# Performance work log

Measured on AMD Instinct MI355X. Metric: run time of the kernel, lower is better.

The kernel has to match this reference:

```python
import jax, jax.numpy as jnp
import numpy as np

N_NODES = 6144
IN_FEATURES = 256
N_HEADS = 4
N_HIDDEN = 64  # out_features, concat=False
LEAKY_SLOPE = 0.2
NEG_INF = -9e16


def setup_inputs() -> dict:
    key = jax.random.key(0)
    k1, k2, k3, k4 = jax.random.split(key, 4)
    h = jax.random.normal(k1, (N_NODES, IN_FEATURES), dtype=jnp.float32)
    adj_mat = jax.random.randint(k2, (N_NODES, N_NODES), 0, 2, dtype=jnp.int32)
    W = jax.random.normal(k3, (IN_FEATURES, N_HEADS * N_HIDDEN), dtype=jnp.float32) * 0.06
    a = jax.random.normal(k4, (N_HEADS, 2 * N_HIDDEN, 1), dtype=jnp.float32) * 0.1
    return {"h": h, "adj_mat": adj_mat, "W": W, "a": a}


def reference(h, adj_mat, W, a):
    n_nodes = h.shape[0]
    # linear transform, dropout is identity in eval mode
    ht = (h @ W).reshape(n_nodes, N_HEADS, N_HIDDEN).transpose(1, 0, 2)  # [H, N, d]
    a_src = a[:, :N_HIDDEN, 0]   # [H, d]
    a_tgt = a[:, N_HIDDEN:, 0]   # [H, d]
    src = jnp.einsum('hnd,hd->hn', ht, a_src)  # [H, N]
    tgt = jnp.einsum('hnd,hd->hn', ht, a_tgt)  # [H, N]
    e = src[:, :, None] + tgt[:, None, :]       # [H, N, N]
    e = jnp.where(e >= 0, e, LEAKY_SLOPE * e)    # leaky relu
    e = jnp.where(adj_mat[None, :, :] > 0, e, jnp.float32(NEG_INF))
    attention = jax.nn.softmax(e, axis=-1)       # [H, N, N]
    h_prime = jnp.einsum('hij,hjd->hid', attention, ht)  # [H, N, d]
    return h_prime.mean(axis=0)                  # [N, d] (concat=False)
```

## Files before the change

kernel.cpp:

```cpp
#include <hip/hip_runtime.h>
#include <hip/hip_bf16.h>

#define N_NODES 6144
#define IN_F 256
#define N_HEADS 4
#define N_HID 64
#define JS 4
#define JLEN (N_NODES / JS)
#define NW (JLEN / 32)
#define SMB_STRIDE 1544

typedef __attribute__((ext_vector_type(4))) float floatx4;
typedef _Float16 half2_t __attribute__((ext_vector_type(2)));
typedef _Float16 half8_t __attribute__((ext_vector_type(8)));
typedef __attribute__((ext_vector_type(4))) unsigned uint4_t;

__global__ __launch_bounds__(256) void ht_gemm_kernel(
    const float* __restrict__ h, const float* __restrict__ W,
    const float* __restrict__ a, short* __restrict__ htF,
    float* __restrict__ srcv, unsigned* __restrict__ tE1pk, unsigned* __restrict__ tE2pk)
{
    __shared__ float As[32][34];
    __shared__ float Bs[32][68];
    __shared__ float redS[32][16];
    __shared__ float redT[32][16];
    __shared__ unsigned short eh1[32], eh2[32];

    const int head = blockIdx.y;
    const int i0 = blockIdx.x * 32;
    const int tid = threadIdx.x;
    const int tx = tid & 15, ty = tid >> 4;

    float acc[2][4] = {};

    for (int k0 = 0; k0 < IN_F; k0 += 32) {
        __syncthreads();
        {
            const int m = tid >> 3, kq = tid & 7;
            const float4 v = *(const float4*)(h + (i0 + m) * IN_F + k0 + kq * 4);
            As[kq*4+0][m] = v.x; As[kq*4+1][m] = v.y;
            As[kq*4+2][m] = v.z; As[kq*4+3][m] = v.w;
        }
        #pragma unroll
        for (int it = 0; it < 2; ++it) {
            int l = it * 256 + tid;
            int k = l >> 4, nq = l & 15;
            *(float4*)&Bs[k][nq*4] = *(const float4*)(W + (k0 + k) * 256 + head * 64 + nq * 4);
        }
        __syncthreads();
        #pragma unroll
        for (int kk = 0; kk < 32; ++kk) {
            const float2 av = *(const float2*)&As[kk][ty*2];
            const float4 bv = *(const float4*)&Bs[kk][tx*4];
            const float aa[2] = {av.x, av.y};
            const float bb[4] = {bv.x, bv.y, bv.z, bv.w};
            #pragma unroll
            for (int r = 0; r < 2; ++r)
                #pragma unroll
                for (int c = 0; c < 4; ++c)
                    acc[r][c] = fmaf(aa[r], bb[c], acc[r][c]);
        }
    }

    #pragma unroll
    for (int r = 0; r < 2; ++r)
        #pragma unroll
        for (int c2 = 0; c2 < 4; ++c2) {
            const int d = tx * 4 + c2;
            const int j = i0 + ty * 2 + r;
            const int jt = j >> 5, q = (j >> 3) & 3, u = j & 7;
            const int c = d >> 4, n = d & 15;
            const size_t F = (((((size_t)head * 192 + jt) * 4 + c) * 16 + n) * 4 + q) * 8 + u;
            const _Float16 hv = (_Float16)acc[r][c2];
            htF[F] = *(const short*)&hv;
        }

    float as_[4], at_[4];
    #pragma unroll
    for (int c = 0; c < 4; ++c) {
        as_[c] = a[head * 128 + tx * 4 + c];
        at_[c] = a[head * 128 + 64 + tx * 4 + c];
    }
    #pragma unroll
    for (int r = 0; r < 2; ++r) {
        float ps = 0.f, pt = 0.f;
        #pragma unroll
        for (int c = 0; c < 4; ++c) {
            ps = fmaf(acc[r][c], as_[c], ps);
            pt = fmaf(acc[r][c], at_[c], pt);
        }
        redS[ty*2+r][tx] = ps;
        redT[ty*2+r][tx] = pt;
    }
    __syncthreads();
    if (tid < 64) {
        const int row = tid & 31;
        const float* src = (tid < 32) ? &redS[row][0] : &redT[row][0];
        float s = 0.f;
        #pragma unroll
        for (int x = 0; x < 16; ++x) s += src[x];
        if (tid < 32) {
            srcv[head * N_NODES + i0 + row] = s;
        } else {
            const _Float16 E1 = (_Float16)__expf(s);
            const _Float16 E2 = (_Float16)__expf(0.2f * s);
            eh1[row] = *(const unsigned short*)&E1;
            eh2[row] = *(const unsigned short*)&E2;
        }
    }
    __syncthreads();
    if (tid < 16) {
        const unsigned v1 = (unsigned)eh1[2*tid] | ((unsigned)eh1[2*tid+1] << 16);
        const unsigned v2 = (unsigned)eh2[2*tid] | ((unsigned)eh2[2*tid+1] << 16);
        tE1pk[head * (N_NODES/2) + i0/2 + tid] = v1;
        tE2pk[head * (N_NODES/2) + i0/2 + tid] = v2;
    }
}

__global__ __launch_bounds__(256) void gat_main_kernel(
    const int* __restrict__ adj, const short* __restrict__ htF,
    const float* __restrict__ srcv, const unsigned* __restrict__ tE1pk,
    const unsigned* __restrict__ tE2pk,
    float* __restrict__ pnum, float* __restrict__ pden)
{
    __shared__ unsigned char smaskB[16 * SMB_STRIDE];

    const int lane = threadIdx.x;
    const int head = threadIdx.y;
    const int jc = blockIdx.y;
    const int i0 = blockIdx.x * 16;
    const int m = lane & 15, quad = lane >> 4;
    const int row = i0 + m;
    const int jbase = jc * JLEN;

    const int tid = head * 64 + lane;
    #pragma unroll
    for (int it = 0; it < 24; ++it) {
        const int flat = it * 256 + tid;
        const int r = flat / 384;
        const int c4 = flat - r * 384;
        const int4 v = *(const int4*)(adj + (size_t)(i0 + r) * N_NODES + jbase + c4 * 4);
        const unsigned b = (unsigned)(v.x | (v.y << 8) | (v.z << 16) | (v.w << 24)) * 255u;
        *(unsigned*)(smaskB + r * SMB_STRIDE + c4 * 4) = b;
    }
    __syncthreads();

    const float sv = srcv[head * N_NODES + row];
    const _Float16 e1h = (_Float16)__expf(sv);
    const _Float16 e2h = (_Float16)__expf(0.2f * sv);
    const half2_t e1s2 = {e1h, e1h};
    const half2_t e2s2 = {e2h, e2h};

    const unsigned* pe1 = tE1pk + head * (N_NODES/2) + (jbase >> 1);
    const unsigned* pe2 = tE2pk + head * (N_NODES/2) + (jbase >> 1);
    const short* fb = htF + ((size_t)(head * 192 + (jbase >> 5)) * 4) * 512 + (m * 4 + quad) * 8;

    half8_t bones;
    #pragma unroll
    for (int u = 0; u < 8; ++u) bones[u] = (_Float16)1.0f;

    floatx4 acc0 = {0,0,0,0}, acc1 = {0,0,0,0}, acc2 = {0,0,0,0}, acc3 = {0,0,0,0};
    floatx4 accD = {0,0,0,0};

    for (int w = 0; w < NW; ++w) {
        const uint4_t E1 = *(const uint4_t*)(pe1 + w * 16 + quad * 4);
        const uint4_t E2 = *(const uint4_t*)(pe2 + w * 16 + quad * 4);
        const unsigned long long mB =
            *(const unsigned long long*)(smaskB + m * SMB_STRIDE + w * 32 + quad * 8);
        const unsigned mlo = (unsigned)mB, mhi = (unsigned)(mB >> 32);

        const half8_t b0 = *(const half8_t*)(fb + (size_t)w * 2048);
        const half8_t b1 = *(const half8_t*)(fb + (size_t)w * 2048 + 512);
        const half8_t b2 = *(const half8_t*)(fb + (size_t)w * 2048 + 1024);
        const half8_t b3 = *(const half8_t*)(fb + (size_t)w * 2048 + 1536);

        const unsigned k0 = __builtin_amdgcn_perm(0u, mlo, 0x01010000u);
        const unsigned k1 = __builtin_amdgcn_perm(0u, mlo, 0x03030202u);
        const unsigned k2 = __builtin_amdgcn_perm(0u, mhi, 0x01010000u);
        const unsigned k3 = __builtin_amdgcn_perm(0u, mhi, 0x03030202u);

        uint4_t af_u;
        #pragma unroll
        for (int p = 0; p < 4; ++p) {
            const unsigned e1u = (p == 0) ? E1.x : (p == 1) ? E1.y : (p == 2) ? E1.z : E1.w;
            const unsigned e2u = (p == 0) ? E2.x : (p == 1) ? E2.y : (p == 2) ? E2.z : E2.w;
            const unsigned ku  = (p == 0) ? k0 : (p == 1) ? k1 : (p == 2) ? k2 : k3;
            const half2_t p1 = __builtin_bit_cast(half2_t, e1u) * e1s2;
            const half2_t p2 = __builtin_bit_cast(half2_t, e2u) * e2s2;
            const half2_t mx = __builtin_elementwise_max(p1, p2);
            const unsigned r = __builtin_bit_cast(unsigned, mx) & ku;
            if (p == 0) af_u.x = r; else if (p == 1) af_u.y = r;
            else if (p == 2) af_u.z = r; else af_u.w = r;
        }
        const half8_t af = __builtin_bit_cast(half8_t, af_u);

        acc0 = __builtin_amdgcn_mfma_f32_16x16x32_f16(af, b0, acc0, 0, 0, 0);
        acc1 = __builtin_amdgcn_mfma_f32_16x16x32_f16(af, b1, acc1, 0, 0, 0);
        acc2 = __builtin_amdgcn_mfma_f32_16x16x32_f16(af, b2, acc2, 0, 0, 0);
        acc3 = __builtin_amdgcn_mfma_f32_16x16x32_f16(af, b3, acc3, 0, 0, 0);
        accD = __builtin_amdgcn_mfma_f32_16x16x32_f16(af, bones, accD, 0, 0, 0);
    }

    const int slot = jc * N_HEADS + head;

    if (m == 0) {
        #pragma unroll
        for (int r = 0; r < 4; ++r)
            pden[slot * N_NODES + i0 + quad * 4 + r] = accD[r];
    }

    #pragma unroll
    for (int r = 0; r < 4; ++r) {
        const int gi = i0 + quad * 4 + r;
        float* np_ = pnum + ((size_t)slot * N_NODES + gi) * N_HID + m;
        np_[0]  = acc0[r];
        np_[16] = acc1[r];
        np_[32] = acc2[r];
        np_[48] = acc3[r];
    }
}

__global__ __launch_bounds__(256) void finalize_kernel(
    const float* __restrict__ pnum, const float* __restrict__ pden,
    float* __restrict__ out)
{
    const int idx = blockIdx.x * 256 + threadIdx.x;
    if (idx >= N_NODES * N_HID) return;
    const int i = idx >> 6;
    const int d = idx & 63;
    float s = 0.f;
    for (int hh = 0; hh < N_HEADS; ++hh) {
        float ns = 0.f, ds = 0.f;
        #pragma unroll
        for (int jc = 0; jc < JS; ++jc) {
            const int slot = jc * N_HEADS + hh;
            ns += pnum[((size_t)slot * N_NODES + i) * N_HID + d];
            ds += pden[slot * N_NODES + i];
        }
        s += ns / ds;
    }
    out[idx] = 0.25f * s;
}

extern "C" void kernel_launch(void* const* d_in, const int* in_sizes, int n_in,
                              void* d_out, int out_size, void* d_ws, size_t ws_size,
                              hipStream_t stream)
{
    const float* h   = (const float*)d_in[0];
    const int*   adj = (const int*)d_in[1];
    const float* W   = (const float*)d_in[2];
    const float* a   = (const float*)d_in[3];
    float* out = (float*)d_out;

    char* ws = (char*)d_ws;
    short* htF = (short*)ws;
    size_t off = (size_t)N_HEADS * N_HID * N_NODES * 2;
    float* srcv = (float*)(ws + off);       off += (size_t)N_HEADS * N_NODES * 4;
    unsigned* tE1pk = (unsigned*)(ws + off); off += (size_t)N_HEADS * (N_NODES/2) * 4;
    unsigned* tE2pk = (unsigned*)(ws + off); off += (size_t)N_HEADS * (N_NODES/2) * 4;
    float* pnum = (float*)(ws + off);        off += (size_t)JS * N_HEADS * N_NODES * N_HID * 4;
    float* pden = (float*)(ws + off);

    ht_gemm_kernel<<<dim3(N_NODES / 32, N_HEADS), 256, 0, stream>>>(h, W, a, htF, srcv, tE1pk, tE2pk);
    gat_main_kernel<<<dim3(N_NODES / 16, JS), dim3(64, 4), 0, stream>>>(
        adj, htF, srcv, tE1pk, tE2pk, pnum, pden);
    finalize_kernel<<<dim3((N_NODES * N_HID) / 256), 256, 0, stream>>>(pnum, pden, out);
}
```

Baseline: 315.6 us.

## Prepack adjacency to bitmask and tile 64 rows per wave per head

Adds a pre-pass that packs the int32 adjacency matrix into 32-bit bitmasks. The main kernel then loads the compact mask into shared memory instead of converting raw ints per block. The main kernel is regridded so each block handles one head and 256 rows, with each wave computing four 16-row tiles. This reuses each loaded htF fragment across four MFMA row tiles. The j-split rises to 8 when workspace allows, which increases partial-sum traffic and register pressure from 20 accumulators in exchange for more parallelism and less redundant feature loading.

```diff
diff --git a/kernel.cpp b/kernel.cpp
--- a/kernel.cpp
+++ b/kernel.cpp
@@ -5,15 +5,35 @@
 #define IN_F 256
 #define N_HEADS 4
 #define N_HID 64
-#define JS 4
-#define JLEN (N_NODES / JS)
-#define NW (JLEN / 32)
-#define SMB_STRIDE 1544
+#define NWORDS (N_NODES / 32)
 
 typedef __attribute__((ext_vector_type(4))) float floatx4;
 typedef _Float16 half2_t __attribute__((ext_vector_type(2)));
 typedef _Float16 half8_t __attribute__((ext_vector_type(8)));
 typedef __attribute__((ext_vector_type(4))) unsigned uint4_t;
+typedef short short2v __attribute__((ext_vector_type(2)));
+
+__global__ __launch_bounds__(256) void pack_adj_kernel(
+    const int* __restrict__ adj, unsigned* __restrict__ mask32)
+{
+    const int waveId = (blockIdx.x * 256 + threadIdx.x) >> 6;
+    const int lane = threadIdx.x & 63;
+    #pragma unroll
+    for (int c = 0; c < 3; ++c) {
+        const size_t W = ((size_t)c * 6144 + waveId) * 64 + lane;
+        const int* p = adj + W * 32;
+        unsigned mw = 0;
+        #pragma unroll
+        for (int k = 0; k < 8; ++k) {
+            const int4 v = *(const int4*)(p + k * 4);
+            mw |= (unsigned)v.x << (k * 4 + 0);
+            mw |= (unsigned)v.y << (k * 4 + 1);
+            mw |= (unsigned)v.z << (k * 4 + 2);
+            mw |= (unsigned)v.w << (k * 4 + 3);
+        }
+        mask32[W] = mw;
+    }
+}
 
 __global__ __launch_bounds__(256) void ht_gemm_kernel(
     const float* __restrict__ h, const float* __restrict__ W,
@@ -117,122 +137,130 @@
     }
 }
 
-__global__ __launch_bounds__(256) void gat_main_kernel(
-    const int* __restrict__ adj, const short* __restrict__ htF,
+__global__ __launch_bounds__(256, 3) void gat_main_kernel(
+    const unsigned* __restrict__ mask32, const short* __restrict__ htF,
     const float* __restrict__ srcv, const unsigned* __restrict__ tE1pk,
     const unsigned* __restrict__ tE2pk,
-    float* __restrict__ pnum, float* __restrict__ pden)
-{
-    __shared__ unsigned char smaskB[16 * SMB_STRIDE];
+    float* __restrict__ pnum, float* __restrict__ pden, int nw)
+{
+    __shared__ unsigned smask[256 * 49];
 
     const int lane = threadIdx.x;
-    const int head = threadIdx.y;
+    const int wy = threadIdx.y;
     const int jc = blockIdx.y;
-    const int i0 = blockIdx.x * 16;
+    const int head = blockIdx.z;
+    const int rb0 = blockIdx.x * 256;
     const int m = lane & 15, quad = lane >> 4;
-    const int row = i0 + m;
-    const int jbase = jc * JLEN;
-
-    const int tid = head * 64 + lane;
-    #pragma unroll
-    for (int it = 0; it < 24; ++it) {
+    const int jbase = jc * nw * 32;
+
+    const int tid = wy * 64 + lane;
+    const int perThread = nw >> 2;
+    for (int it = 0; it < perThread; ++it) {
         const int flat = it * 256 + tid;
-        const int r = flat / 384;
-        const int c4 = flat - r * 384;
-        const int4 v = *(const int4*)(adj + (size_t)(i0 + r) * N_NODES + jbase + c4 * 4);
-        const unsigned b = (unsigned)(v.x | (v.y << 8) | (v.z << 16) | (v.w << 24)) * 255u;
-        *(unsigned*)(smaskB + r * SMB_STRIDE + c4 * 4) = b;
+        const int r = flat / perThread, w4 = flat % perThread;
+        const uint4_t v = *(const uint4_t*)(mask32 + (size_t)(rb0 + r) * NWORDS + jc * nw + w4 * 4);
+        unsigned* dst = &smask[r * 49 + w4 * 4];
+        dst[0] = v.x; dst[1] = v.y; dst[2] = v.z; dst[3] = v.w;
     }
     __syncthreads();
 
-    const float sv = srcv[head * N_NODES + row];
-    const _Float16 e1h = (_Float16)__expf(sv);
-    const _Float16 e2h = (_Float16)__expf(0.2f * sv);
-    const half2_t e1s2 = {e1h, e1h};
-    const half2_t e2s2 = {e2h, e2h};
+    const int rowbase = rb0 + wy * 64;
+    half2_t e1s[4], e2s[4];
+    #pragma unroll
+    for (int t = 0; t < 4; ++t) {
+        const float sv = srcv[head * N_NODES + rowbase + t * 16 + m];
+        const _Float16 a1 = (_Float16)__expf(sv);
+        const _Float16 a2 = (_Float16)__expf(0.2f * sv);
+        e1s[t] = (half2_t){a1, a1};
+        e2s[t] = (half2_t){a2, a2};
+    }
 
     const unsigned* pe1 = tE1pk + head * (N_NODES/2) + (jbase >> 1);
     const unsigned* pe2 = tE2pk + head * (N_NODES/2) + (jbase >> 1);
     const short* fb = htF + ((size_t)(head * 192 + (jbase >> 5)) * 4) * 512 + (m * 4 + quad) * 8;
+    const unsigned* mrow = &smask[(wy * 64 + m) * 49];
 
     half8_t bones;
     #pragma unroll
     for (int u = 0; u < 8; ++u) bones[u] = (_Float16)1.0f;
 
-    floatx4 acc0 = {0,0,0,0}, acc1 = {0,0,0,0}, acc2 = {0,0,0,0}, acc3 = {0,0,0,0};
-    floatx4 accD = {0,0,0,0};
-
-    for (int w = 0; w < NW; ++w) {
+    floatx4 accN[4][4];
+    floatx4 accD[4];
+    #pragma unroll
+    for (int t = 0; t < 4; ++t) {
+        accD[t] = (floatx4){0,0,0,0};
+        #pragma unroll
+        for (int c = 0; c < 4; ++c) accN[t][c] = (floatx4){0,0,0,0};
+    }
+
+    for (int w = 0; w < nw; ++w) {
         const uint4_t E1 = *(const uint4_t*)(pe1 + w * 16 + quad * 4);
         const uint4_t E2 = *(const uint4_t*)(pe2 + w * 16 + quad * 4);
-        const unsigned long long mB =
-            *(const unsigned long long*)(smaskB + m * SMB_STRIDE + w * 32 + quad * 8);
-        const unsigned mlo = (unsigned)mB, mhi = (unsigned)(mB >> 32);
-
-        const half8_t b0 = *(const half8_t*)(fb + (size_t)w * 2048);
-        const half8_t b1 = *(const half8_t*)(fb + (size_t)w * 2048 + 512);
-        const half8_t b2 = *(const half8_t*)(fb + (size_t)w * 2048 + 1024);
-        const half8_t b3 = *(const half8_t*)(fb + (size_t)w * 2048 + 1536);
-
-        const unsigned k0 = __builtin_amdgcn_perm(0u, mlo, 0x01010000u);
-        const unsigned k1 = __builtin_amdgcn_perm(0u, mlo, 0x03030202u);
-        const unsigned k2 = __builtin_amdgcn_perm(0u, mhi, 0x01010000u);
-        const unsigned k3 = __builtin_amdgcn_perm(0u, mhi, 0x03030202u);
-
-        uint4_t af_u;
-        #pragma unroll
-        for (int p = 0; p < 4; ++p) {
-            const unsigned e1u = (p == 0) ? E1.x : (p == 1) ? E1.y : (p == 2) ? E1.z : E1.w;
-            const unsigned e2u = (p == 0) ? E2.x : (p == 1) ? E2.y : (p == 2) ? E2.z : E2.w;
-            const unsigned ku  = (p == 0) ? k0 : (p == 1) ? k1 : (p == 2) ? k2 : k3;
-            const half2_t p1 = __builtin_bit_cast(half2_t, e1u) * e1s2;
-            const half2_t p2 = __builtin_bit_cast(half2_t, e2u) * e2s2;
-            const half2_t mx = __builtin_elementwise_max(p1, p2);
-            const unsigned r = __builtin_bit_cast(unsigned, mx) & ku;
-            if (p == 0) af_u.x = r; else if (p == 1) af_u.y = r;
-            else if (p == 2) af_u.z = r; else af_u.w = r;
-        }
-        const half8_t af = __builtin_bit_cast(half8_t, af_u);
-
-        acc0 = __builtin_amdgcn_mfma_f32_16x16x32_f16(af, b0, acc0, 0, 0, 0);
-        acc1 = __builtin_amdgcn_mfma_f32_16x16x32_f16(af, b1, acc1, 0, 0, 0);
-        acc2 = __builtin_amdgcn_mfma_f32_16x16x32_f16(af, b2, acc2, 0, 0, 0);
-        acc3 = __builtin_amdgcn_mfma_f32_16x16x32_f16(af, b3, acc3, 0, 0, 0);
-        accD = __builtin_amdgcn_mfma_f32_16x16x32_f16(af, bones, accD, 0, 0, 0);
+        const unsigned E1a[4] = {E1.x, E1.y, E1.z, E1.w};
+        const unsigned E2a[4] = {E2.x, E2.y, E2.z, E2.w};
+        half8_t b[4];
+        #pragma unroll
+        for (int c = 0; c < 4; ++c)
+            b[c] = *(const half8_t*)(fb + (size_t)w * 2048 + c * 512);
+
+        #pragma unroll
+        for (int t = 0; t < 4; ++t) {
+            const unsigned bits = (mrow[t * (16*49) + w] >> (quad * 8)) & 0xffu;
+            const short2v tt = __builtin_bit_cast(short2v, bits * 0x10001u);
+            uint4_t af_u;
+            #pragma unroll
+            for (int p = 0; p < 4; ++p) {
+                const short2v shl = (p == 0) ? (short2v){15,14} : (p == 1) ? (short2v){13,12}
+                                 : (p == 2) ? (short2v){11,10} : (short2v){9,8};
+                const short2v k = (tt << shl) >> (short2v){15,15};
+                const half2_t p1 = __builtin_bit_cast(half2_t, E1a[p]) * e1s[t];
+                const half2_t p2 = __builtin_bit_cast(half2_t, E2a[p]) * e2s[t];
+                const half2_t mx = __builtin_elementwise_max(p1, p2);
+                const unsigned r = __builtin_bit_cast(unsigned, mx) & __builtin_bit_cast(unsigned, k);
+                if (p == 0) af_u.x = r; else if (p == 1) af_u.y = r;
+                else if (p == 2) af_u.z = r; else af_u.w = r;
+            }
+            const half8_t af = __builtin_bit_cast(half8_t, af_u);
+            #pragma unroll
+            for (int c = 0; c < 4; ++c)
+                accN[t][c] = __builtin_amdgcn_mfma_f32_16x16x32_f16(af, b[c], accN[t][c], 0, 0, 0);
+            accD[t] = __builtin_amdgcn_mfma_f32_16x16x32_f16(af, bones, accD[t], 0, 0, 0);
+        }
     }
 
     const int slot = jc * N_HEADS + head;
-
-    if (m == 0) {
-        #pragma unroll
-        for (int r = 0; r < 4; ++r)
-            pden[slot * N_NODES + i0 + quad * 4 + r] = accD[r];
-    }
-
-    #pragma unroll
-    for (int r = 0; r < 4; ++r) {
-        const int gi = i0 + quad * 4 + r;
-        float* np_ = pnum + ((size_t)slot * N_NODES + gi) * N_HID + m;
-        np_[0]  = acc0[r];
-        np_[16] = acc1[r];
-        np_[32] = acc2[r];
-        np_[48] = acc3[r];
+    #pragma unroll
+    for (int t = 0; t < 4; ++t) {
+        if (m == 0) {
+            #pragma unroll
+            for (int r = 0; r < 4; ++r)
+                pden[slot * N_NODES + rowbase + t * 16 + quad * 4 + r] = accD[t][r];
+        }
+        #pragma unroll
+        for (int r = 0; r < 4; ++r) {
+            const int gi = rowbase + t * 16 + quad * 4 + r;
+            float* np_ = pnum + ((size_t)slot * N_NODES + gi) * N_HID + m;
+            np_[0]  = accN[t][0][r];
+            np_[16] = accN[t][1][r];
+            np_[32] = accN[t][2][r];
+            np_[48] = accN[t][3][r];
+        }
     }
 }
 
 __global__ __launch_bounds__(256) void finalize_kernel(
     const float* __restrict__ pnum, const float* __restrict__ pden,
-    float* __restrict__ out)
+    float* __restrict__ out, int js)
 {
     const int idx = blockIdx.x * 256 + threadIdx.x;
     if (idx >= N_NODES * N_HID) return;
     const int i = idx >> 6;
     const int d = idx & 63;
     float s = 0.f;
+    #pragma unroll
     for (int hh = 0; hh < N_HEADS; ++hh) {
         float ns = 0.f, ds = 0.f;
-        #pragma unroll
-        for (int jc = 0; jc < JS; ++jc) {
+        for (int jc = 0; jc < js; ++jc) {
             const int slot = jc * N_HEADS + hh;
             ns += pnum[((size_t)slot * N_NODES + i) * N_HID + d];
             ds += pden[slot * N_NODES + i];
@@ -255,14 +283,22 @@
     char* ws = (char*)d_ws;
     short* htF = (short*)ws;
     size_t off = (size_t)N_HEADS * N_HID * N_NODES * 2;
-    float* srcv = (float*)(ws + off);       off += (size_t)N_HEADS * N_NODES * 4;
+    float* srcv = (float*)(ws + off);        off += (size_t)N_HEADS * N_NODES * 4;
     unsigned* tE1pk = (unsigned*)(ws + off); off += (size_t)N_HEADS * (N_NODES/2) * 4;
     unsigned* tE2pk = (unsigned*)(ws + off); off += (size_t)N_HEADS * (N_NODES/2) * 4;
-    float* pnum = (float*)(ws + off);        off += (size_t)JS * N_HEADS * N_NODES * N_HID * 4;
+    unsigned* mask32 = (unsigned*)(ws + off); off += (size_t)N_NODES * NWORDS * 4;
+
+    const size_t per_js = (size_t)N_HEADS * N_NODES * N_HID * 4 + (size_t)N_HEADS * N_NODES * 4;
+    int js = 8;
+    if (off + 8 * per_js > ws_size) js = 4;
+    const int nw = (N_NODES / js) / 32;
+
+    float* pnum = (float*)(ws + off);        off += (size_t)js * N_HEADS * N_NODES * N_HID * 4;
     float* pden = (float*)(ws + off);
 
+    pack_adj_kernel<<<1536, 256, 0, stream>>>(adj, mask32);
     ht_gemm_kernel<<<dim3(N_NODES / 32, N_HEADS), 256, 0, stream>>>(h, W, a, htF, srcv, tE1pk, tE2pk);
-    gat_main_kernel<<<dim3(N_NODES / 16, JS), dim3(64, 4), 0, stream>>>(
-        adj, htF, srcv, tE1pk, tE2pk, pnum, pden);
-    finalize_kernel<<<dim3((N_NODES * N_HID) / 256), 256, 0, stream>>>(pnum, pden, out);
-}
+    gat_main_kernel<<<dim3(N_NODES / 256, js, N_HEADS), dim3(64, 4), 0, stream>>>(
+        mask32, htF, srcv, tE1pk, tE2pk, pnum, pden, nw);
+    finalize_kernel<<<dim3((N_NODES * N_HID) / 256), 256, 0, stream>>>(pnum, pden, out, js);
+}
```

Result: faster. 282.8 us (-10.4%).
